# Performance work log

Hardware: AMD Instinct MI355X
Metric: run time of the kernel (lower is better)

Reference implementation:

```python
import jax, jax.numpy as jnp
import numpy as np

NUM_HEADS = 8
MAX_POINTS = 8


def _sample_one(img, x, y):
    # img: [hd, Hs, Ws]; x, y: [N, P] pixel coords. Bilinear, zeros padding,
    # align_corners=True (caller already converted normalized coords to pixels).
    Hs, Ws = img.shape[-2], img.shape[-1]
    x0f = jnp.floor(x); y0f = jnp.floor(y)
    x0 = x0f.astype(jnp.int32); y0 = y0f.astype(jnp.int32)
    x1 = x0 + 1; y1 = y0 + 1
    wx1 = x - x0f; wx0 = 1.0 - wx1
    wy1 = y - y0f; wy0 = 1.0 - wy1

    def gather(yi, xi):
        valid = ((yi >= 0) & (yi < Hs) & (xi >= 0) & (xi < Ws)).astype(img.dtype)
        yc = jnp.clip(yi, 0, Hs - 1)
        xc = jnp.clip(xi, 0, Ws - 1)
        return img[:, yc, xc] * valid  # [hd, N, P]

    return (gather(y0, x0) * (wy0 * wx0) + gather(y0, x1) * (wy0 * wx1)
            + gather(y1, x0) * (wy1 * wx0) + gather(y1, x1) * (wy1 * wx1))


def _forward(query, ref, q_w, q_b, kv_w, kv_b, off_w, off_b, out_w, out_b, H, W, n_points):
    B, N, C = query.shape
    hd = C // NUM_HEADS
    scale = hd ** -0.5

    q = (query @ q_w + q_b).reshape(B, N, NUM_HEADS, hd)
    # kv_proj is dead code in the source forward (k, v are never used); params kept for parity.

    offsets = (query @ off_w + off_b).reshape(B, N, NUM_HEADS, MAX_POINTS, 2)
    offsets = offsets[:, :, :, :n_points]  # [B, N, nh, P, 2]

    ys = jnp.arange(H, dtype=query.dtype)
    xs = jnp.arange(W, dtype=query.dtype)
    coords = jnp.stack(jnp.meshgrid(ys, xs, indexing='ij'), -1).reshape(N, 2)  # (y, x)
    loc = coords[None, :, None, None, :] + offsets  # [B, N, nh, P, 2]
    g0 = loc[..., 0] / (H - 1) * 2.0 - 1.0
    g1 = loc[..., 1] / (W - 1) * 2.0 - 1.0
    # grid_sample reads grid[...,0] as x and grid[...,1] as y -> faithful to the
    # source's coordinate-channel ordering (channel 0 was normalized with H).
    x_pix = (g0 + 1.0) * 0.5 * (W - 1)
    y_pix = (g1 + 1.0) * 0.5 * (H - 1)

    ref_img = ref.reshape(B, C, H, W)  # faithful to source's .view (raw reinterpret, no permute)
    ref_heads = ref_img.reshape(B, NUM_HEADS, hd, H, W)  # per-head channel slice

    xb = x_pix.transpose(0, 2, 1, 3)  # [B, nh, N, P]
    yb = y_pix.transpose(0, 2, 1, 3)
    sampled = jax.vmap(jax.vmap(_sample_one))(ref_heads, xb, yb)  # [B, nh, hd, N, P]
    sampled = sampled.transpose(0, 3, 1, 4, 2)  # [B, N, nh, P, hd]

    attn = jax.nn.softmax(jnp.einsum('bnhd,bnhpd->bnhp', q, sampled) * scale, axis=-1)
    out = jnp.einsum('bnhp,bnhpd->bnhd', attn, sampled).reshape(B, N, C)
    return out @ out_w + out_b


def setup_inputs():
    key = jax.random.key(0)
    B, H, W, C = 4, 64, 64, 512
    N = H * W
    ks = jax.random.split(key, 8)
    w = lambda k, shp: jax.random.normal(k, shp, jnp.float32) * 0.02
    return {
        'query': jax.random.normal(ks[0], (B, N, C), jnp.float32),
        'ref': jax.random.normal(ks[1], (B, N, C), jnp.float32),
        'q_w': w(ks[2], (C, C)), 'q_b': jnp.zeros((C,), jnp.float32),
        'kv_w': w(ks[3], (C, 2 * C)), 'kv_b': jnp.zeros((2 * C,), jnp.float32),
        'off_w': w(ks[4], (C, NUM_HEADS * MAX_POINTS * 2)),
        'off_b': jnp.zeros((NUM_HEADS * MAX_POINTS * 2,), jnp.float32),
        'out_w': w(ks[5], (C, C)), 'out_b': jnp.zeros((C,), jnp.float32),
        'H': H, 'W': W, 'n_points': 8,
    }


def reference(query, ref, q_w, q_b, kv_w, kv_b, off_w, off_b, out_w, out_b, H, W, n_points):
    return _forward(query, ref, q_w, q_b, kv_w, kv_b, off_w, off_b, out_w, out_b, H, W, n_points)
```

## Files before the change

kernel.cpp:

```cpp
#include <hip/hip_runtime.h>
#include <cmath>

#define NUM_HEADS 8
#define MAX_POINTS 8
#define HD 64

typedef short bf16x8 __attribute__((ext_vector_type(8)));
typedef float f32x4 __attribute__((ext_vector_type(4)));

typedef const __attribute__((address_space(1))) unsigned int gu32;
typedef __attribute__((address_space(3))) unsigned int lu32;

__device__ __forceinline__ unsigned short f2bf(float f) {
    unsigned u = __float_as_uint(f);
    unsigned r = (u + 0x7fff + ((u >> 16) & 1)) >> 16;
    return (unsigned short)r;
}
__device__ __forceinline__ unsigned packbf2(float a, float b) {
    return (unsigned)f2bf(a) | ((unsigned)f2bf(b) << 16);
}
__device__ __forceinline__ void unpack8(uint4 u, float* f) {
    f[0] = __uint_as_float(u.x << 16); f[1] = __uint_as_float(u.x & 0xffff0000u);
    f[2] = __uint_as_float(u.y << 16); f[3] = __uint_as_float(u.y & 0xffff0000u);
    f[4] = __uint_as_float(u.z << 16); f[5] = __uint_as_float(u.z & 0xffff0000u);
    f[6] = __uint_as_float(u.w << 16); f[7] = __uint_as_float(u.w & 0xffff0000u);
}

__global__ __launch_bounds__(256) void cvt_bf16_k(
    const float* __restrict__ in, unsigned short* __restrict__ out, int n)
{
    int i = (blockIdx.x * 256 + threadIdx.x) * 4;
    if (i >= n) return;
    float4 v = *(const float4*)&in[i];
    ushort4 o;
    o.x = f2bf(v.x); o.y = f2bf(v.y); o.z = f2bf(v.z); o.w = f2bf(v.w);
    *(ushort4*)&out[i] = o;
}

__global__ __launch_bounds__(256) void tconv_k(
    const float* __restrict__ in, unsigned short* __restrict__ out, int K, int N)
{
    __shared__ float tile[32][33];
    size_t ib = (size_t)blockIdx.z * K * N;
    int k0 = blockIdx.x * 32, n0 = blockIdx.y * 32;
    int tx = threadIdx.x, ty = threadIdx.y;
#pragma unroll
    for (int i = 0; i < 32; i += 8)
        tile[ty + i][tx] = in[ib + (size_t)(k0 + ty + i) * N + n0 + tx];
    __syncthreads();
#pragma unroll
    for (int i = 0; i < 32; i += 8)
        out[ib + (size_t)(n0 + ty + i) * K + k0 + tx] = f2bf(tile[tx][ty + i]);
}

__global__ __launch_bounds__(256) void tconvW_k(
    const float* __restrict__ q_w, const float* __restrict__ off_w,
    const float* __restrict__ out_w, unsigned short* __restrict__ wcat,
    unsigned short* __restrict__ woutT)
{
    const float* in; unsigned short* out; int N;
    int z = blockIdx.z;
    if (z == 0)      { in = q_w;   out = wcat;             N = 512; }
    else if (z == 1) { in = off_w; out = wcat + 512 * 512; N = 128;
                       if (blockIdx.y >= 4) return; }
    else             { in = out_w; out = woutT;            N = 512; }
    __shared__ float tile[32][33];
    int k0 = blockIdx.x * 32, n0 = blockIdx.y * 32;
    int tx = threadIdx.x, ty = threadIdx.y;
#pragma unroll
    for (int i = 0; i < 32; i += 8)
        tile[ty + i][tx] = in[(size_t)(k0 + ty + i) * N + n0 + tx];
    __syncthreads();
#pragma unroll
    for (int i = 0; i < 32; i += 8)
        out[(size_t)(n0 + ty + i) * 512 + k0 + tx] = f2bf(tile[tx][ty + i]);
}

__device__ __forceinline__ void gemm128_core(
    const unsigned short* A, const unsigned short* BT, int K,
    int bm, int bn, int tid, unsigned short* As, unsigned short* Bs,
    f32x4 (&acc)[4][4])
{
    int wave = tid >> 6, lane = tid & 63;
    int quad = lane >> 4, l16 = lane & 15;
    int wm = (wave >> 1) * 64, wn = (wave & 1) * 64;
    int srow = tid >> 2, sq = (tid & 3) * 8;
    const unsigned short* aP0 = &A[(size_t)(bm + srow) * K + sq];
    const unsigned short* aP1 = aP0 + (size_t)64 * K;
    const unsigned short* bP0 = &BT[(size_t)(bn + srow) * K + sq];
    const unsigned short* bP1 = bP0 + (size_t)64 * K;
    lu32* aL0 = (lu32*)&As[wave * 512];
    lu32* aL1 = (lu32*)&As[2048 + wave * 512];
    lu32* bL0 = (lu32*)&Bs[wave * 512];
    lu32* bL1 = (lu32*)&Bs[2048 + wave * 512];

    for (int k0 = 0; k0 < K; k0 += 32) {
        __builtin_amdgcn_global_load_lds((gu32*)(aP0 + k0), aL0, 16, 0, 0);
        __builtin_amdgcn_global_load_lds((gu32*)(aP1 + k0), aL1, 16, 0, 0);
        __builtin_amdgcn_global_load_lds((gu32*)(bP0 + k0), bL0, 16, 0, 0);
        __builtin_amdgcn_global_load_lds((gu32*)(bP1 + k0), bL1, 16, 0, 0);
        __syncthreads();
        bf16x8 af[4], bfr[4];
#pragma unroll
        for (int t = 0; t < 4; ++t) {
            af[t]  = *(const bf16x8*)&As[(wm + t * 16 + l16) * 32 + quad * 8];
            bfr[t] = *(const bf16x8*)&Bs[(wn + t * 16 + l16) * 32 + quad * 8];
        }
#pragma unroll
        for (int mt = 0; mt < 4; ++mt)
#pragma unroll
            for (int nt = 0; nt < 4; ++nt)
                acc[mt][nt] = __builtin_amdgcn_mfma_f32_16x16x32_bf16(
                    af[mt], bfr[nt], acc[mt][nt], 0, 0, 0);
        __syncthreads();
    }
}

__global__ __launch_bounds__(256) void gemm_qoff_k(
    const unsigned short* __restrict__ A, const unsigned short* __restrict__ BT,
    const float* __restrict__ q_b, const float* __restrict__ off_b,
    unsigned short* __restrict__ qout, float* __restrict__ offout,
    int M, int K)
{
    __shared__ unsigned short As[128 * 32];
    __shared__ unsigned short Bs[128 * 32];
    int tid = threadIdx.x;
    int wave = tid >> 6, lane = tid & 63;
    int quad = lane >> 4, l16 = lane & 15;
    int bm = blockIdx.y * 128, bn = blockIdx.x * 128;
    int wm = (wave >> 1) * 64, wn = (wave & 1) * 64;

    f32x4 acc[4][4];
#pragma unroll
    for (int i = 0; i < 4; ++i)
#pragma unroll
        for (int j = 0; j < 4; ++j) acc[i][j] = (f32x4){0.f, 0.f, 0.f, 0.f};

    gemm128_core(A, BT, K, bm, bn, tid, As, Bs, acc);

#pragma unroll
    for (int mt = 0; mt < 4; ++mt)
#pragma unroll
        for (int nt = 0; nt < 4; ++nt) {
            int r0 = bm + wm + mt * 16 + quad * 4;
            int c  = bn + wn + nt * 16 + l16;
            if (bn < 512) {
                float bv = q_b[c];
#pragma unroll
                for (int r = 0; r < 4; ++r)
                    qout[(size_t)(r0 + r) * 512 + c] = f2bf(acc[mt][nt][r] + bv);
            } else {
                int co = c - 512;
                float bv = off_b[co];
#pragma unroll
                for (int r = 0; r < 4; ++r)
                    offout[(size_t)(r0 + r) * 128 + co] = acc[mt][nt][r] + bv;
            }
        }
}

__global__ __launch_bounds__(256) void gemm_out_k(
    const unsigned short* __restrict__ A, const unsigned short* __restrict__ BT,
    const float* __restrict__ bias, float* __restrict__ Cf, int M, int N, int K)
{
    __shared__ unsigned short As[128 * 32];
    __shared__ unsigned short Bs[128 * 32];
    int tid = threadIdx.x;
    int wave = tid >> 6, lane = tid & 63;
    int quad = lane >> 4, l16 = lane & 15;
    int bm = blockIdx.y * 128, bn = blockIdx.x * 128;
    int wm = (wave >> 1) * 64, wn = (wave & 1) * 64;

    f32x4 acc[4][4];
#pragma unroll
    for (int i = 0; i < 4; ++i)
#pragma unroll
        for (int j = 0; j < 4; ++j) acc[i][j] = (f32x4){0.f, 0.f, 0.f, 0.f};

    gemm128_core(A, BT, K, bm, bn, tid, As, Bs, acc);

#pragma unroll
    for (int mt = 0; mt < 4; ++mt)
#pragma unroll
        for (int nt = 0; nt < 4; ++nt) {
            int r0 = bm + wm + mt * 16 + quad * 4;
            int c  = bn + wn + nt * 16 + l16;
            float bv = bias[c];
#pragma unroll
            for (int r = 0; r < 4; ++r)
                Cf[(size_t)(r0 + r) * N + c] = acc[mt][nt][r] + bv;
        }
}

__global__ __launch_bounds__(256) void sample_attn8_k(
    const unsigned short* __restrict__ qb, const float* __restrict__ offb,
    const unsigned short* __restrict__ refT, unsigned short* __restrict__ ob,
    const int* __restrict__ npp)
{
    int npts = *npp;
    int bn = blockIdx.x * 4 + (threadIdx.x >> 6);
    int lane = threadIdx.x & 63;
    int h = lane >> 3;
    int c8 = (lane & 7) << 3;
    int coff = (h << 6) + c8;
    int b = bn >> 12;
    int n = bn & 4095;
    int row = n >> 6, col = n & 63;

    float qv[8];
    unpack8(*(const uint4*)&qb[(bn << 9) + coff], qv);

    const float* op = offb + (bn << 7) + (h << 4);
    const unsigned short* rb = refT + ((size_t)b << 21) + coff;

    unsigned svp[MAX_POINTS][4];
    float lg[MAX_POINTS];
#pragma unroll
    for (int p = 0; p < MAX_POINTS; ++p) {
        float2 o2 = *(const float2*)(op + p * 2);
        float x = (float)row + o2.x;
        float y = (float)col + o2.y;
        float x0f = floorf(x), y0f = floorf(y);
        int x0 = (int)x0f, y0 = (int)y0f;
        float wx1 = x - x0f, wx0 = 1.f - wx1;
        float wy1 = y - y0f, wy0 = 1.f - wy1;
        float wt[4] = {wy0 * wx0, wy0 * wx1, wy1 * wx0, wy1 * wx1};

        float a8[8] = {0.f, 0.f, 0.f, 0.f, 0.f, 0.f, 0.f, 0.f};
#pragma unroll
        for (int t = 0; t < 4; ++t) {
            int yi = y0 + (t >> 1);
            int xi = x0 + (t & 1);
            bool ok = ((unsigned)yi < 64u) & ((unsigned)xi < 64u);
            float wv = ok ? wt[t] : 0.f;
            int yc = min(max(yi, 0), 63);
            int xc = min(max(xi, 0), 63);
            float sf[8];
            unpack8(*(const uint4*)&rb[((yc << 6) + xc) << 9], sf);
#pragma unroll
            for (int j = 0; j < 8; ++j) a8[j] = fmaf(wv, sf[j], a8[j]);
        }
        float t = 0.f;
#pragma unroll
        for (int j = 0; j < 8; ++j) t = fmaf(qv[j], a8[j], t);
        t += __shfl_xor(t, 1);
        t += __shfl_xor(t, 2);
        t += __shfl_xor(t, 4);
        lg[p] = (p < npts) ? t * 0.125f : -1e30f;

        svp[p][0] = packbf2(a8[0], a8[1]);
        svp[p][1] = packbf2(a8[2], a8[3]);
        svp[p][2] = packbf2(a8[4], a8[5]);
        svp[p][3] = packbf2(a8[6], a8[7]);
    }

    float mx = -1e30f;
#pragma unroll
    for (int p = 0; p < MAX_POINTS; ++p) mx = fmaxf(mx, lg[p]);
    float ssum = 0.f;
#pragma unroll
    for (int p = 0; p < MAX_POINTS; ++p) {
        lg[p] = __expf(lg[p] - mx);
        ssum += lg[p];
    }
    float inv = 1.f / ssum;

    float o8[8] = {0.f, 0.f, 0.f, 0.f, 0.f, 0.f, 0.f, 0.f};
#pragma unroll
    for (int p = 0; p < MAX_POINTS; ++p) {
#pragma unroll
        for (int j = 0; j < 4; ++j) {
            o8[2 * j + 0] = fmaf(lg[p], __uint_as_float(svp[p][j] << 16), o8[2 * j + 0]);
            o8[2 * j + 1] = fmaf(lg[p], __uint_as_float(svp[p][j] & 0xffff0000u), o8[2 * j + 1]);
        }
    }

    uint4 o;
    o.x = packbf2(o8[0] * inv, o8[1] * inv);
    o.y = packbf2(o8[2] * inv, o8[3] * inv);
    o.z = packbf2(o8[4] * inv, o8[5] * inv);
    o.w = packbf2(o8[6] * inv, o8[7] * inv);
    *(uint4*)&ob[(bn << 9) + coff] = o;
}

extern "C" void kernel_launch(void* const* d_in, const int* in_sizes, int n_in,
                              void* d_out, int out_size, void* d_ws, size_t ws_size,
                              hipStream_t stream) {
    const float* query = (const float*)d_in[0];
    const float* ref   = (const float*)d_in[1];
    const float* q_w   = (const float*)d_in[2];
    const float* q_b   = (const float*)d_in[3];
    const float* off_w = (const float*)d_in[6];
    const float* off_b = (const float*)d_in[7];
    const float* out_w = (const float*)d_in[8];
    const float* out_b = (const float*)d_in[9];
    const int* npp  = (const int*)d_in[12];

    const int C = 512;
    const int B = 4;
    const int N = 64 * 64;
    const int M = B * N;
    const int OFFD = NUM_HEADS * MAX_POINTS * 2;

    float* offbuf = (float*)d_ws;
    unsigned short* refT_bf = (unsigned short*)(offbuf + (size_t)M * OFFD);
    unsigned short* qin_bf  = refT_bf + (size_t)M * C;
    unsigned short* qbuf_bf = qin_bf  + (size_t)M * C;
    unsigned short* obuf_bf = qbuf_bf + (size_t)M * C;
    unsigned short* wcat    = obuf_bf + (size_t)M * C;
    unsigned short* woutT   = wcat + (size_t)(C + OFFD) * C;

    dim3 blk(256);
    cvt_bf16_k<<<dim3((M * C) / 1024), blk, 0, stream>>>(query, qin_bf, M * C);
    tconvW_k<<<dim3(16, 16, 3), dim3(32, 8), 0, stream>>>(
        q_w, off_w, out_w, wcat, woutT);
    tconv_k<<<dim3(C / 32, N / 32, B), dim3(32, 8), 0, stream>>>(ref, refT_bf, C, N);

    gemm_qoff_k<<<dim3(5, M / 128), blk, 0, stream>>>(
        qin_bf, wcat, q_b, off_b, qbuf_bf, offbuf, M, C);

    sample_attn8_k<<<dim3(M / 4), blk, 0, stream>>>(
        qbuf_bf, offbuf, refT_bf, obuf_bf, npp);

    gemm_out_k<<<dim3(C / 128, M / 128), blk, 0, stream>>>(
        obuf_bf, woutT, out_b, (float*)d_out, M, C, C);
}
```

Baseline: 218.3 us.

## Split sampling points across two waves per query with LDS softmax exchange

The sampling/attention kernel now uses two wavefronts per query, each handling four of the eight sampling points, so each block covers two queries instead of four. Logits are exchanged through shared memory for the softmax, and the partial weighted sums are reduced across the two waves through LDS. Block indices are remapped to interleave queries across batches. The aim is more parallelism and less register pressure per thread for the latency-bound gather, at the cost of two block barriers, extra LDS traffic and twice as many blocks.

```diff
diff --git a/kernel.cpp b/kernel.cpp
--- a/kernel.cpp
+++ b/kernel.cpp
@@ -192,31 +192,41 @@
         }
 }
 
-__global__ __launch_bounds__(256) void sample_attn8_k(
+__global__ __launch_bounds__(256) void sample_attn_sp_k(
     const unsigned short* __restrict__ qb, const float* __restrict__ offb,
     const unsigned short* __restrict__ refT, unsigned short* __restrict__ ob,
     const int* __restrict__ npp)
 {
+    __shared__ float slog[2][NUM_HEADS][MAX_POINTS];
+    __shared__ float spart[2][8][64];
     int npts = *npp;
-    int bn = blockIdx.x * 4 + (threadIdx.x >> 6);
-    int lane = threadIdx.x & 63;
+    int tid = threadIdx.x;
+    int qsel = tid >> 7;
+    int w = (tid >> 6) & 1;
+    int lane = tid & 63;
     int h = lane >> 3;
-    int c8 = (lane & 7) << 3;
+    int j = lane & 7;
+    int c8 = j << 3;
     int coff = (h << 6) + c8;
-    int b = bn >> 12;
-    int n = bn & 4095;
+
+    int bi = blockIdx.x;
+    int grp = bi & 7;
+    int b = grp >> 1;
+    int idx = ((bi >> 3) << 1) | (grp & 1);
+    int n = (idx << 1) | qsel;
+    int bn = (b << 12) | n;
     int row = n >> 6, col = n & 63;
 
     float qv[8];
     unpack8(*(const uint4*)&qb[(bn << 9) + coff], qv);
 
-    const float* op = offb + (bn << 7) + (h << 4);
+    const float* op = offb + (bn << 7) + (h << 4) + (w << 3);
     const unsigned short* rb = refT + ((size_t)b << 21) + coff;
 
-    unsigned svp[MAX_POINTS][4];
-    float lg[MAX_POINTS];
-#pragma unroll
-    for (int p = 0; p < MAX_POINTS; ++p) {
+    float sv[4][8];
+    float lg[4];
+#pragma unroll
+    for (int p = 0; p < 4; ++p) {
         float2 o2 = *(const float2*)(op + p * 2);
         float x = (float)row + o2.x;
         float y = (float)col + o2.y;
@@ -238,49 +248,58 @@
             float sf[8];
             unpack8(*(const uint4*)&rb[((yc << 6) + xc) << 9], sf);
 #pragma unroll
-            for (int j = 0; j < 8; ++j) a8[j] = fmaf(wv, sf[j], a8[j]);
+            for (int k = 0; k < 8; ++k) a8[k] = fmaf(wv, sf[k], a8[k]);
         }
         float t = 0.f;
 #pragma unroll
-        for (int j = 0; j < 8; ++j) t = fmaf(qv[j], a8[j], t);
+        for (int k = 0; k < 8; ++k) {
+            sv[p][k] = a8[k];
+            t = fmaf(qv[k], a8[k], t);
+        }
         t += __shfl_xor(t, 1);
         t += __shfl_xor(t, 2);
         t += __shfl_xor(t, 4);
-        lg[p] = (p < npts) ? t * 0.125f : -1e30f;
-
-        svp[p][0] = packbf2(a8[0], a8[1]);
-        svp[p][1] = packbf2(a8[2], a8[3]);
-        svp[p][2] = packbf2(a8[4], a8[5]);
-        svp[p][3] = packbf2(a8[6], a8[7]);
-    }
-
+        lg[p] = ((w * 4 + p) < npts) ? t * 0.125f : -1e30f;
+    }
+
+    slog[qsel][h][w * 4 + (j & 3)] = lg[j & 3];
+    __syncthreads();
+
+    float l8[8];
+#pragma unroll
+    for (int k = 0; k < 8; ++k) l8[k] = slog[qsel][h][k];
     float mx = -1e30f;
 #pragma unroll
-    for (int p = 0; p < MAX_POINTS; ++p) mx = fmaxf(mx, lg[p]);
+    for (int k = 0; k < 8; ++k) mx = fmaxf(mx, l8[k]);
     float ssum = 0.f;
 #pragma unroll
-    for (int p = 0; p < MAX_POINTS; ++p) {
-        lg[p] = __expf(lg[p] - mx);
-        ssum += lg[p];
+    for (int k = 0; k < 8; ++k) {
+        l8[k] = __expf(l8[k] - mx);
+        ssum += l8[k];
     }
     float inv = 1.f / ssum;
 
-    float o8[8] = {0.f, 0.f, 0.f, 0.f, 0.f, 0.f, 0.f, 0.f};
-#pragma unroll
-    for (int p = 0; p < MAX_POINTS; ++p) {
-#pragma unroll
-        for (int j = 0; j < 4; ++j) {
-            o8[2 * j + 0] = fmaf(lg[p], __uint_as_float(svp[p][j] << 16), o8[2 * j + 0]);
-            o8[2 * j + 1] = fmaf(lg[p], __uint_as_float(svp[p][j] & 0xffff0000u), o8[2 * j + 1]);
-        }
-    }
-
-    uint4 o;
-    o.x = packbf2(o8[0] * inv, o8[1] * inv);
-    o.y = packbf2(o8[2] * inv, o8[3] * inv);
-    o.z = packbf2(o8[4] * inv, o8[5] * inv);
-    o.w = packbf2(o8[6] * inv, o8[7] * inv);
-    *(uint4*)&ob[(bn << 9) + coff] = o;
+    float o8[8];
+#pragma unroll
+    for (int k = 0; k < 8; ++k)
+        o8[k] = l8[w * 4 + 0] * sv[0][k] + l8[w * 4 + 1] * sv[1][k]
+              + l8[w * 4 + 2] * sv[2][k] + l8[w * 4 + 3] * sv[3][k];
+
+    if (w == 1) {
+#pragma unroll
+        for (int k = 0; k < 8; ++k) spart[qsel][k][lane] = o8[k];
+    }
+    __syncthreads();
+    if (w == 0) {
+#pragma unroll
+        for (int k = 0; k < 8; ++k) o8[k] += spart[qsel][k][lane];
+        uint4 o;
+        o.x = packbf2(o8[0] * inv, o8[1] * inv);
+        o.y = packbf2(o8[2] * inv, o8[3] * inv);
+        o.z = packbf2(o8[4] * inv, o8[5] * inv);
+        o.w = packbf2(o8[6] * inv, o8[7] * inv);
+        *(uint4*)&ob[(bn << 9) + coff] = o;
+    }
 }
 
 extern "C" void kernel_launch(void* const* d_in, const int* in_sizes, int n_in,
@@ -319,7 +338,7 @@
     gemm_qoff_k<<<dim3(5, M / 128), blk, 0, stream>>>(
         qin_bf, wcat, q_b, off_b, qbuf_bf, offbuf, M, C);
 
-    sample_attn8_k<<<dim3(M / 4), blk, 0, stream>>>(
+    sample_attn_sp_k<<<dim3(M / 2), blk, 0, stream>>>(
         qbuf_bf, offbuf, refT_bf, obuf_bf, npp);
 
     gemm_out_k<<<dim3(C / 128, M / 128), blk, 0, stream>>>(
```

Result: faster. 212.4 us (-2.7%).
